# Kernel tuning notes

Measured on AMD Instinct MI355X. Metric: run time of the kernel, lower is better.

The kernel has to match this reference:

```python
import jax, jax.numpy as jnp
import numpy as np

NSIDE = 64
NLAT = 4 * NSIDE - 1        # 255 iso-latitude rings
NLON = 4 * NSIDE            # 256 = max pixels per ring
NPIX = 12 * NSIDE * NSIDE   # 49152 HEALPix pixels
LMAX = NLAT                 # 255
MMAX = NLON // 2 + 1        # 129
BATCH, CHAN = 8, 32


def _ring_geometry():
    # HEALPix ring scheme: ring r (0-based), 1-based i=r+1
    #  north cap i<nside: nph=4i, phi shift 0.5
    #  equatorial nside<=i<=3*nside: nph=4*nside, shift alternates {0,0.5}
    #  south cap: mirror of north cap
    nph = np.zeros(NLAT, np.int64)
    shift = np.zeros(NLAT, np.float64)
    for r in range(NLAT):
        i = r + 1
        if i < NSIDE:
            nph[r], shift[r] = 4 * i, 0.5
        elif i <= 3 * NSIDE:
            nph[r], shift[r] = 4 * NSIDE, 0.5 * ((i - NSIDE + 1) % 2)
        else:
            nph[r], shift[r] = 4 * (NLAT - r), 0.5
    offs = np.concatenate([[0], np.cumsum(nph)[:-1]])
    p = np.arange(NLON)
    mask = (p[None, :] < nph[:, None])                       # [nlat, nlon]
    idx = (offs[:, None] + p[None, :]) * mask                # padded -> 0
    phase = 2.0 * np.pi * (p[None, :] + shift[:, None]) / nph[:, None] * mask
    return idx.astype(np.int32), mask.astype(np.float32), phase.astype(np.float32)


def setup_inputs() -> dict:
    key = jax.random.key(0)
    k1, k2, k3 = jax.random.split(key, 3)
    idx, mask, phase = _ring_geometry()
    x = jax.random.normal(k1, (BATCH, CHAN, NPIX), jnp.float32)
    pct = jax.random.normal(k2, (MMAX, LMAX, NLAT), jnp.float32) * 0.1  # Legendre table stand-in
    w = jax.random.uniform(k3, (NLAT,), jnp.float32)                    # per-ring quadrature weights
    return {"x": x, "pct": pct, "w": w,
            "ring_index": jnp.asarray(idx),
            "ring_mask": jnp.asarray(mask),
            "phase": jnp.asarray(phase)}


def _healpix_rfft_real(x, ring_index, ring_mask, phase):
    # x: [..., npix] -> per-ring DFT coefficients as real pairs [..., nlat, mmax, 2]
    rings = x[..., ring_index] * ring_mask                 # [..., nlat, nlon]
    m = jnp.arange(MMAX, dtype=phase.dtype)
    ang = phase[:, :, None] * m                            # [nlat, nlon, mmax]
    fr = jnp.einsum('...kp,kpm->...km', rings, jnp.cos(ang))
    fi = -jnp.einsum('...kp,kpm->...km', rings, jnp.sin(ang))
    return jnp.stack([fr, fi], axis=-1)                    # n=2 is view_as_real axis


def reference(x, pct, w, ring_index, ring_mask, phase):
    # healpix ring rFFT, then Legendre contraction (einsum '...kmn,mlk->...lmn')
    f = _healpix_rfft_real(x, ring_index, ring_mask, phase)  # [..., nlat, mmax, 2]
    weights = pct * w                                        # [mmax, lmax, nlat]
    out = jnp.einsum('...kmn,mlk->...lmn', f, weights)       # [..., lmax, mmax, 2]
    return out
```

## Files before the change

### kernel.cpp

```cpp
#include <hip/hip_runtime.h>

#define NLAT 255
#define NLON 256
#define NPIX 49152
#define MMAX 129
#define MCS  258
#define NTBL 65
#define TROWS 264

typedef unsigned short ushort_t;
typedef __attribute__((ext_vector_type(8)))  short  bf16x8;
typedef __attribute__((ext_vector_type(4)))  short  short4v;
typedef __attribute__((ext_vector_type(16))) float  f32x16;
typedef __attribute__((ext_vector_type(4)))  float  float4v;
typedef __attribute__((ext_vector_type(4), aligned(4))) float float4u;

__device__ __forceinline__ ushort_t f2bf(float f) {
    union { float f; unsigned u; } v; v.f = f;
    unsigned r = v.u + 0x7FFFu + ((v.u >> 16) & 1u);
    return (ushort_t)(r >> 16);
}
__device__ __forceinline__ float bf2f(ushort_t h) {
    union { unsigned u; float f; } v; v.u = ((unsigned)h) << 16;
    return v.f;
}

__global__ __launch_bounds__(256) void trigK(const float* __restrict__ phase,
                                             const float* __restrict__ mask,
                                             ushort_t* __restrict__ Ttab2) {
    const int tt  = blockIdx.x;
    const int mcs = blockIdx.y;
    const int p   = threadIdx.x;
    const int r   = (tt < 63) ? tt : (tt == 63 ? 63 : 64);
    float val = 0.f;
    if (mcs < MCS) {
        float ph = phase[r * NLON + p];
        float mk = mask[r * NLON + p];
        float fm = (float)(mcs >> 1);
        float s, c;
        __sincosf(ph * fm, &s, &c);
        val = (mcs & 1) ? (-s * mk) : (c * mk);
    }
    Ttab2[(((size_t)tt * 4 + (p >> 6)) * TROWS + mcs) * 64 + (p & 63)] = f2bf(val);
}

__global__ __launch_bounds__(512, 2) void stageA(const float* __restrict__ x,
                                                 const int* __restrict__ ring_index,
                                                 const ushort_t* __restrict__ Ttab2,
                                                 ushort_t* __restrict__ f1) {
    __shared__ __align__(16) ushort_t Rs[256 * 72];
    __shared__ __align__(16) ushort_t Ts[TROWS * 72];

    const int r  = blockIdx.x;
    const int i1 = r + 1;
    const int nph = (i1 < 64) ? 4 * i1 : (i1 <= 192 ? 256 : 4 * (256 - i1));
    const int tbl = (i1 < 64) ? r : (i1 <= 192 ? (63 + (((i1 - 63) & 1) ^ 1)) : 254 - r);
    const int base = ring_index[r * NLON];

    const int t    = threadIdx.x;
    const int lane = t & 63;
    const int wid  = t >> 6;
    const int wrow = wid >> 1, wcol = wid & 1;
    const int lg   = lane >> 5;
    const int lc   = lane & 31;

    f32x16 acc[5][2];
#pragma unroll
    for (int tau = 0; tau < 5; ++tau)
#pragma unroll
        for (int i = 0; i < 2; ++i)
#pragma unroll
            for (int q = 0; q < 16; ++q) acc[tau][i][q] = 0.f;

    for (int pc = 0; pc < nph; pc += 64) {
        {
            const int p0 = (t & 15) * 4;
            const bool ok = (pc + p0) < nph;
#pragma unroll
            for (int pass = 0; pass < 8; ++pass) {
                int bc = (t >> 4) + pass * 32;
                float4v v = {0.f, 0.f, 0.f, 0.f};
                if (ok) v = *(const float4v*)(x + (size_t)bc * NPIX + base + pc + p0);
                short4v h;
                h[0] = (short)f2bf(v[0]); h[1] = (short)f2bf(v[1]);
                h[2] = (short)f2bf(v[2]); h[3] = (short)f2bf(v[3]);
                *(short4v*)(Rs + bc * 72 + p0) = h;
            }
        }
        {
            const ushort_t* slab = Ttab2 + ((size_t)tbl * 4 + (pc >> 6)) * (TROWS * 64);
#pragma unroll
            for (int pass = 0; pass < 5; ++pass) {
                int id = t + pass * 512;
                if (id < (TROWS * 64 / 8)) {
                    bf16x8 v = *(const bf16x8*)(slab + id * 8);
                    *(bf16x8*)(Ts + (id >> 3) * 72 + (id & 7) * 8) = v;
                }
            }
        }
        __syncthreads();
#pragma unroll
        for (int ks = 0; ks < 4; ++ks) {
            bf16x8 a0 = *(const bf16x8*)(Rs + (wrow * 64 + lc) * 72 + ks * 16 + lg * 8);
            bf16x8 a1 = *(const bf16x8*)(Rs + (wrow * 64 + 32 + lc) * 72 + ks * 16 + lg * 8);
#pragma unroll
            for (int tau = 0; tau < 5; ++tau) {
                int rr = tau * 64 + wcol * 32 + lc;
                int trow = rr > (TROWS - 1) ? (TROWS - 1) : rr;
                bf16x8 b = *(const bf16x8*)(Ts + trow * 72 + ks * 16 + lg * 8);
                acc[tau][0] = __builtin_amdgcn_mfma_f32_32x32x16_bf16(a0, b, acc[tau][0], 0, 0, 0);
                acc[tau][1] = __builtin_amdgcn_mfma_f32_32x32x16_bf16(a1, b, acc[tau][1], 0, 0, 0);
            }
        }
        __syncthreads();
    }

    ushort_t* Olds = Rs;
#pragma unroll
    for (int tau = 0; tau < 5; ++tau) {
        __syncthreads();
        {
            const int mcsl = wcol * 32 + lc;
#pragma unroll
            for (int i = 0; i < 2; ++i)
#pragma unroll
                for (int q = 0; q < 16; ++q) {
                    int bc = wrow * 64 + i * 32 + 4 * lg + (q & 3) + 8 * (q >> 2);
                    Olds[mcsl * 264 + bc] = f2bf(acc[tau][i][q]);
                }
        }
        __syncthreads();
#pragma unroll
        for (int it = 0; it < 4; ++it) {
            int row = (t >> 5) + it * 16;
            int ch  = t & 31;
            int mcs = tau * 64 + row;
            if (mcs < MCS) {
                bf16x8 v = *(const bf16x8*)(Olds + row * 264 + ch * 8);
                int m = mcs >> 1, n = mcs & 1;
                *(bf16x8*)(f1 + ((size_t)m * NLAT + r) * 512 + n * 256 + ch * 8) = v;
            }
        }
    }
}

__global__ __launch_bounds__(256) void transK(const ushort_t* __restrict__ f1,
                                              ushort_t* __restrict__ f1t, int m0) {
    __shared__ __align__(16) ushort_t T[64][72];
    const int m  = m0 + blockIdx.x;
    const int k0 = blockIdx.y * 64;
    const int b0 = blockIdx.z * 64;
    const int t  = threadIdx.x;
#pragma unroll
    for (int it = 0; it < 2; ++it) {
        int id = t + it * 256;
        int kk = id >> 3, ch = id & 7;
        int k  = k0 + kk;
        bf16x8 v = {0,0,0,0,0,0,0,0};
        if (k < NLAT)
            v = *(const bf16x8*)(f1 + ((size_t)m * NLAT + k) * 512 + b0 + ch * 8);
        *(bf16x8*)(&T[kk][ch * 8]) = v;
    }
    __syncthreads();
#pragma unroll
    for (int it = 0; it < 2; ++it) {
        int id  = t + it * 256;
        int bb  = id & 63, ch8 = id >> 6;
        bf16x8 v;
#pragma unroll
        for (int j = 0; j < 8; ++j) v[j] = T[ch8 * 8 + j][bb];
        *(bf16x8*)(f1t + ((size_t)m * 512 + b0 + bb) * 256 + k0 + ch8 * 8) = v;
    }
}

__global__ __launch_bounds__(256) void stageB(const ushort_t* __restrict__ f1t,
                                              const float* __restrict__ pct,
                                              const float* __restrict__ w,
                                              ushort_t* __restrict__ otmp,
                                              int mbase) {
    __shared__ __align__(16) ushort_t SB[17408];
    ushort_t* WsB = SB;
    ushort_t* EsB = SB;

    int m, sub;
    if (mbase == 0) { m = blockIdx.x >> 3; sub = blockIdx.x & 7; }
    else {
        int id = blockIdx.x;
        m = mbase + ((id >> 6) << 3) + (id & 7);
        sub = (id >> 3) & 7;
        if (m >= MMAX) return;
    }
    const int b2t = (sub & 3) * 128;
    const int lt  = (sub >> 2) * 128;

    const int t    = threadIdx.x;
    const int lane = t & 63;
    const int wid  = t >> 6;
    const int wrow = wid >> 1, wcol = wid & 1;
    const int lg   = lane >> 5, lc = lane & 31;

    const int flr   = t >> 1;
    const int fhalf = t & 1;
    const int gl    = lt + flr;

    f32x16 acc[2][2];
#pragma unroll
    for (int i = 0; i < 2; ++i)
#pragma unroll
        for (int j = 0; j < 2; ++j)
#pragma unroll
            for (int q = 0; q < 16; ++q) acc[i][j][q] = 0.f;

    const ushort_t* arow0 = f1t + ((size_t)m * 512 + b2t + wrow * 64 + lc) * 256;
    const ushort_t* arow1 = arow0 + 32 * 256;

    auto fill = [&](ushort_t* buf, int kc) {
        const int kb = kc + fhalf * 16;
        float vals[16];
        if (gl < NLAT) {
            const float* src = pct + ((size_t)m * NLAT + gl) * NLAT + kb;
#pragma unroll
            for (int c = 0; c < 4; ++c) {
                int k4 = kb + c * 4;
                if (k4 + 4 <= NLAT) {
                    float4u pv = *(const float4u*)(src + c * 4);
                    float4v wv = *(const float4v*)(w + k4);
#pragma unroll
                    for (int j = 0; j < 4; ++j) vals[c * 4 + j] = pv[j] * wv[j];
                } else {
#pragma unroll
                    for (int j = 0; j < 4; ++j) {
                        int k = k4 + j;
                        vals[c * 4 + j] = (k < NLAT) ? src[c * 4 + j] * w[k] : 0.f;
                    }
                }
            }
        } else {
#pragma unroll
            for (int c = 0; c < 16; ++c) vals[c] = 0.f;
        }
        ushort_t* dst = buf + flr * 40 + fhalf * 16;
#pragma unroll
        for (int c = 0; c < 4; ++c) {
            short4v h;
            h[0] = (short)f2bf(vals[c * 4 + 0]);
            h[1] = (short)f2bf(vals[c * 4 + 1]);
            h[2] = (short)f2bf(vals[c * 4 + 2]);
            h[3] = (short)f2bf(vals[c * 4 + 3]);
            *(short4v*)(dst + c * 4) = h;
        }
    };

    fill(WsB, 0);
    __syncthreads();
    int buf = 0;
    for (int kc = 0; kc < 256; kc += 32, buf ^= 1) {
        if (kc + 32 < 256) fill(WsB + (buf ^ 1) * 5120, kc + 32);
        const ushort_t* W = WsB + buf * 5120;
#pragma unroll
        for (int ks = 0; ks < 2; ++ks) {
            const int kb = kc + ks * 16 + lg * 8;
            bf16x8 b0 = *(const bf16x8*)(W + (wcol * 64 + lc) * 40 + ks * 16 + lg * 8);
            bf16x8 b1 = *(const bf16x8*)(W + (wcol * 64 + 32 + lc) * 40 + ks * 16 + lg * 8);
            bf16x8 a0 = *(const bf16x8*)(arow0 + kb);
            bf16x8 a1 = *(const bf16x8*)(arow1 + kb);
            acc[0][0] = __builtin_amdgcn_mfma_f32_32x32x16_bf16(a0, b0, acc[0][0], 0, 0, 0);
            acc[0][1] = __builtin_amdgcn_mfma_f32_32x32x16_bf16(a0, b1, acc[0][1], 0, 0, 0);
            acc[1][0] = __builtin_amdgcn_mfma_f32_32x32x16_bf16(a1, b0, acc[1][0], 0, 0, 0);
            acc[1][1] = __builtin_amdgcn_mfma_f32_32x32x16_bf16(a1, b1, acc[1][1], 0, 0, 0);
        }
        __syncthreads();
    }

#pragma unroll
    for (int i = 0; i < 2; ++i)
#pragma unroll
        for (int jj = 0; jj < 2; ++jj) {
            int ll = wcol * 64 + jj * 32 + lc;
#pragma unroll
            for (int q = 0; q < 16; ++q) {
                int bl = wrow * 64 + i * 32 + 4 * lg + (q & 3) + 8 * (q >> 2);
                EsB[bl * 136 + ll] = f2bf(acc[i][jj][q]);
            }
        }
    __syncthreads();
#pragma unroll
    for (int it = 0; it < 8; ++it) {
        int id2 = t + it * 256;
        int row = id2 >> 4, ch = id2 & 15;
        bf16x8 v = *(const bf16x8*)(EsB + row * 136 + ch * 8);
        *(bf16x8*)(otmp + (((size_t)m * 512 + b2t + row) << 8) + lt + ch * 8) = v;
    }
}

__global__ __launch_bounds__(256) void permuteK(const ushort_t* __restrict__ otmp,
                                                float* __restrict__ out) {
    __shared__ ushort_t L[MCS * 66];
    const int bc = blockIdx.x;
    const int l0 = blockIdx.y * 64;
    const int t  = threadIdx.x;
    const int ll = t & 63;
    const int l  = l0 + ll;
#pragma unroll 4
    for (int it = 0; it < 65; ++it) {
        int mn = (t >> 6) + it * 4;
        if (mn < MCS) {
            int mm = mn >> 1, n = mn & 1;
            ushort_t v = 0;
            if (l < NLAT)
                v = otmp[(((size_t)mm * 512 + n * 256 + bc) << 8) + l];
            L[mn * 66 + ll] = v;
        }
    }
    __syncthreads();
    for (int ll2 = 0; ll2 < 64; ++ll2) {
        int lo = l0 + ll2;
        if (lo >= NLAT) break;
        size_t rowb = ((size_t)bc * NLAT + lo) * MCS;
        out[rowb + t] = bf2f(L[t * 66 + ll2]);
        if (t < 2)
            out[rowb + 256 + t] = bf2f(L[(256 + t) * 66 + ll2]);
    }
}

extern "C" void kernel_launch(void* const* d_in, const int* in_sizes, int n_in,
                              void* d_out, int out_size, void* d_ws, size_t ws_size,
                              hipStream_t stream) {
    const float* x          = (const float*)d_in[0];
    const float* pct        = (const float*)d_in[1];
    const float* w          = (const float*)d_in[2];
    const int*   ring_index = (const int*)d_in[3];
    const float* ring_mask  = (const float*)d_in[4];
    const float* phase      = (const float*)d_in[5];
    float* out = (float*)d_out;

    char* wsb = (char*)d_ws;
    ushort_t* f1    = (ushort_t*)wsb;
    ushort_t* Ttab2 = (ushort_t*)(wsb + 33684480);
    ushort_t* f1t   = (ushort_t*)(wsb + 33552384);
    ushort_t* otmp  = (ushort_t*)wsb;

    trigK   <<<dim3(NTBL, TROWS), 256, 0, stream>>>(phase, ring_mask, Ttab2);
    stageA  <<<dim3(NLAT),      512, 0, stream>>>(x, ring_index, Ttab2, f1);
    transK  <<<dim3(1, 4, 8),   256, 0, stream>>>(f1, f1t, 128);
    transK  <<<dim3(128, 4, 8), 256, 0, stream>>>(f1, f1t, 0);
    stageB  <<<dim3(16),        256, 0, stream>>>(f1t, pct, w, otmp, 0);
    stageB  <<<dim3(1024),      256, 0, stream>>>(f1t, pct, w, otmp, 2);
    permuteK<<<dim3(256, 4),    256, 0, stream>>>(otmp, out);
}
```

Measured before the change: 135.7 us.

## Enlarge stageB tile to full l range and stage A operand in LDS

```diff
diff --git a/kernel.cpp b/kernel.cpp
--- a/kernel.cpp
+++ b/kernel.cpp
@@ -173,123 +173,139 @@
     }
 }
 
-__global__ __launch_bounds__(256) void stageB(const ushort_t* __restrict__ f1t,
-                                              const float* __restrict__ pct,
-                                              const float* __restrict__ w,
-                                              ushort_t* __restrict__ otmp,
-                                              int mbase) {
-    __shared__ __align__(16) ushort_t SB[17408];
-    ushort_t* WsB = SB;
-    ushort_t* EsB = SB;
+__global__ __launch_bounds__(256, 2) void stageB(const ushort_t* __restrict__ f1t,
+                                                 const float* __restrict__ pct,
+                                                 const float* __restrict__ w,
+                                                 ushort_t* __restrict__ otmp,
+                                                 int mbase) {
+    __shared__ __align__(16) ushort_t SB[30720];
+    ushort_t* As = SB;
+    ushort_t* Ws = SB + 10240;
+    ushort_t* Es = SB;
 
     int m, sub;
-    if (mbase == 0) { m = blockIdx.x >> 3; sub = blockIdx.x & 7; }
+    if (mbase == 0) { m = blockIdx.x >> 2; sub = blockIdx.x & 3; }
     else {
-        int id = blockIdx.x;
-        m = mbase + ((id >> 6) << 3) + (id & 7);
-        sub = (id >> 3) & 7;
-        if (m >= MMAX) return;
-    }
-    const int b2t = (sub & 3) * 128;
-    const int lt  = (sub >> 2) * 128;
-
-    const int t    = threadIdx.x;
-    const int lane = t & 63;
-    const int wid  = t >> 6;
-    const int wrow = wid >> 1, wcol = wid & 1;
-    const int lg   = lane >> 5, lc = lane & 31;
-
-    const int flr   = t >> 1;
-    const int fhalf = t & 1;
-    const int gl    = lt + flr;
-
-    f32x16 acc[2][2];
+        int mm = ((blockIdx.x >> 5) << 3) | (blockIdx.x & 7);
+        if (mm > 126) return;
+        m = mbase + mm;
+        sub = (blockIdx.x >> 3) & 3;
+    }
+    const int b2t = sub * 128;
+
+    const int t     = threadIdx.x;
+    const int lane  = t & 63;
+    const int wid   = t >> 6;
+    const int wrow  = wid >> 1, wlcol = wid & 1;
+    const int lg    = lane >> 5, lc = lane & 31;
+
+    f32x16 acc[2][4];
 #pragma unroll
     for (int i = 0; i < 2; ++i)
 #pragma unroll
-        for (int j = 0; j < 2; ++j)
+        for (int j = 0; j < 4; ++j)
 #pragma unroll
             for (int q = 0; q < 16; ++q) acc[i][j][q] = 0.f;
 
-    const ushort_t* arow0 = f1t + ((size_t)m * 512 + b2t + wrow * 64 + lc) * 256;
-    const ushort_t* arow1 = arow0 + 32 * 256;
-
-    auto fill = [&](ushort_t* buf, int kc) {
-        const int kb = kc + fhalf * 16;
-        float vals[16];
-        if (gl < NLAT) {
-            const float* src = pct + ((size_t)m * NLAT + gl) * NLAT + kb;
-#pragma unroll
-            for (int c = 0; c < 4; ++c) {
-                int k4 = kb + c * 4;
-                if (k4 + 4 <= NLAT) {
-                    float4u pv = *(const float4u*)(src + c * 4);
-                    float4v wv = *(const float4v*)(w + k4);
-#pragma unroll
-                    for (int j = 0; j < 4; ++j) vals[c * 4 + j] = pv[j] * wv[j];
-                } else {
-#pragma unroll
-                    for (int j = 0; j < 4; ++j) {
-                        int k = k4 + j;
-                        vals[c * 4 + j] = (k < NLAT) ? src[c * 4 + j] * w[k] : 0.f;
+    auto fillA = [&](ushort_t* dst, int kc) {
+#pragma unroll
+        for (int pass = 0; pass < 2; ++pass) {
+            int id  = t + pass * 256;
+            int row = id >> 2, ch = id & 3;
+            bf16x8 v = *(const bf16x8*)(f1t + ((size_t)m * 512 + b2t + row) * 256 + kc + ch * 8);
+            *(bf16x8*)(dst + row * 40 + ch * 8) = v;
+        }
+    };
+    auto fillW = [&](ushort_t* dst, int kc) {
+#pragma unroll
+        for (int pass = 0; pass < 2; ++pass) {
+            int id   = t + pass * 256;
+            int lrow = id >> 1, half = id & 1;
+            int kb   = kc + half * 16;
+            float vals[16];
+            if (lrow < NLAT) {
+                const float* src = pct + ((size_t)m * NLAT + lrow) * NLAT + kb;
+#pragma unroll
+                for (int c = 0; c < 4; ++c) {
+                    int k4 = kb + c * 4;
+                    if (k4 + 4 <= NLAT) {
+                        float4u pv = *(const float4u*)(src + c * 4);
+                        float4v wv = *(const float4v*)(w + k4);
+#pragma unroll
+                        for (int j = 0; j < 4; ++j) vals[c * 4 + j] = pv[j] * wv[j];
+                    } else {
+#pragma unroll
+                        for (int j = 0; j < 4; ++j) {
+                            int k = k4 + j;
+                            vals[c * 4 + j] = (k < NLAT) ? src[c * 4 + j] * w[k] : 0.f;
+                        }
                     }
                 }
-            }
-        } else {
-#pragma unroll
-            for (int c = 0; c < 16; ++c) vals[c] = 0.f;
-        }
-        ushort_t* dst = buf + flr * 40 + fhalf * 16;
-#pragma unroll
-        for (int c = 0; c < 4; ++c) {
-            short4v h;
-            h[0] = (short)f2bf(vals[c * 4 + 0]);
-            h[1] = (short)f2bf(vals[c * 4 + 1]);
-            h[2] = (short)f2bf(vals[c * 4 + 2]);
-            h[3] = (short)f2bf(vals[c * 4 + 3]);
-            *(short4v*)(dst + c * 4) = h;
+            } else {
+#pragma unroll
+                for (int c = 0; c < 16; ++c) vals[c] = 0.f;
+            }
+            ushort_t* d = dst + lrow * 40 + half * 16;
+#pragma unroll
+            for (int c = 0; c < 4; ++c) {
+                short4v h;
+                h[0] = (short)f2bf(vals[c * 4 + 0]);
+                h[1] = (short)f2bf(vals[c * 4 + 1]);
+                h[2] = (short)f2bf(vals[c * 4 + 2]);
+                h[3] = (short)f2bf(vals[c * 4 + 3]);
+                *(short4v*)(d + c * 4) = h;
+            }
         }
     };
 
-    fill(WsB, 0);
+    fillA(As, 0);
+    fillW(Ws, 0);
     __syncthreads();
     int buf = 0;
     for (int kc = 0; kc < 256; kc += 32, buf ^= 1) {
-        if (kc + 32 < 256) fill(WsB + (buf ^ 1) * 5120, kc + 32);
-        const ushort_t* W = WsB + buf * 5120;
+        if (kc + 32 < 256) {
+            fillA(As + (buf ^ 1) * 5120, kc + 32);
+            fillW(Ws + (buf ^ 1) * 10240, kc + 32);
+        }
+        const ushort_t* A = As + buf * 5120;
+        const ushort_t* W = Ws + buf * 10240;
 #pragma unroll
         for (int ks = 0; ks < 2; ++ks) {
-            const int kb = kc + ks * 16 + lg * 8;
-            bf16x8 b0 = *(const bf16x8*)(W + (wcol * 64 + lc) * 40 + ks * 16 + lg * 8);
-            bf16x8 b1 = *(const bf16x8*)(W + (wcol * 64 + 32 + lc) * 40 + ks * 16 + lg * 8);
-            bf16x8 a0 = *(const bf16x8*)(arow0 + kb);
-            bf16x8 a1 = *(const bf16x8*)(arow1 + kb);
-            acc[0][0] = __builtin_amdgcn_mfma_f32_32x32x16_bf16(a0, b0, acc[0][0], 0, 0, 0);
-            acc[0][1] = __builtin_amdgcn_mfma_f32_32x32x16_bf16(a0, b1, acc[0][1], 0, 0, 0);
-            acc[1][0] = __builtin_amdgcn_mfma_f32_32x32x16_bf16(a1, b0, acc[1][0], 0, 0, 0);
-            acc[1][1] = __builtin_amdgcn_mfma_f32_32x32x16_bf16(a1, b1, acc[1][1], 0, 0, 0);
-        }
-        __syncthreads();
-    }
-
-#pragma unroll
-    for (int i = 0; i < 2; ++i)
-#pragma unroll
-        for (int jj = 0; jj < 2; ++jj) {
-            int ll = wcol * 64 + jj * 32 + lc;
-#pragma unroll
-            for (int q = 0; q < 16; ++q) {
-                int bl = wrow * 64 + i * 32 + 4 * lg + (q & 3) + 8 * (q >> 2);
-                EsB[bl * 136 + ll] = f2bf(acc[i][jj][q]);
-            }
-        }
-    __syncthreads();
-#pragma unroll
-    for (int it = 0; it < 8; ++it) {
-        int id2 = t + it * 256;
-        int row = id2 >> 4, ch = id2 & 15;
-        bf16x8 v = *(const bf16x8*)(EsB + row * 136 + ch * 8);
-        *(bf16x8*)(otmp + (((size_t)m * 512 + b2t + row) << 8) + lt + ch * 8) = v;
+            const int ko = ks * 16 + lg * 8;
+            bf16x8 a0 = *(const bf16x8*)(A + (wrow * 64 + lc) * 40 + ko);
+            bf16x8 a1 = *(const bf16x8*)(A + (wrow * 64 + 32 + lc) * 40 + ko);
+#pragma unroll
+            for (int jj = 0; jj < 4; ++jj) {
+                bf16x8 b = *(const bf16x8*)(W + (wlcol * 128 + jj * 32 + lc) * 40 + ko);
+                acc[0][jj] = __builtin_amdgcn_mfma_f32_32x32x16_bf16(a0, b, acc[0][jj], 0, 0, 0);
+                acc[1][jj] = __builtin_amdgcn_mfma_f32_32x32x16_bf16(a1, b, acc[1][jj], 0, 0, 0);
+            }
+        }
+        __syncthreads();
+    }
+
+#pragma unroll
+    for (int h = 0; h < 2; ++h) {
+        if (h) __syncthreads();
+        if (wlcol == h) {
+#pragma unroll
+            for (int i = 0; i < 2; ++i)
+#pragma unroll
+                for (int jj = 0; jj < 4; ++jj)
+#pragma unroll
+                    for (int q = 0; q < 16; ++q) {
+                        int bl = wrow * 64 + i * 32 + 4 * lg + (q & 3) + 8 * (q >> 2);
+                        Es[bl * 136 + jj * 32 + lc] = f2bf(acc[i][jj][q]);
+                    }
+        }
+        __syncthreads();
+#pragma unroll
+        for (int it = 0; it < 8; ++it) {
+            int id  = t + it * 256;
+            int row = id >> 4, ch = id & 15;
+            bf16x8 v = *(const bf16x8*)(Es + row * 136 + ch * 8);
+            *(bf16x8*)(otmp + (((size_t)m * 512 + b2t + row) << 8) + h * 128 + ch * 8) = v;
+        }
     }
 }
 
@@ -344,7 +360,7 @@
     stageA  <<<dim3(NLAT),      512, 0, stream>>>(x, ring_index, Ttab2, f1);
     transK  <<<dim3(1, 4, 8),   256, 0, stream>>>(f1, f1t, 128);
     transK  <<<dim3(128, 4, 8), 256, 0, stream>>>(f1, f1t, 0);
-    stageB  <<<dim3(16),        256, 0, stream>>>(f1t, pct, w, otmp, 0);
-    stageB  <<<dim3(1024),      256, 0, stream>>>(f1t, pct, w, otmp, 2);
+    stageB  <<<dim3(8),         256, 0, stream>>>(f1t, pct, w, otmp, 0);
+    stageB  <<<dim3(544),       256, 0, stream>>>(f1t, pct, w, otmp, 2);
     permuteK<<<dim3(256, 4),    256, 0, stream>>>(otmp, out);
 }
```

Result: no change. 137.8 us (+1.5%).
